# Kernel tuning notes

Hardware: AMD Instinct MI355X
Metric: run time of the kernel (lower is better)

## Reference

```python
import jax, jax.numpy as jnp
import numpy as np

B, T, H, Z0, D, MH = 1024, 256, 128, 64, 8, 256  # batch, time_steps, hidden, init_noise, data, mlp width


def _p(k, shape):
    s = 1.0 / np.sqrt(shape[0])
    return jax.random.uniform(k, shape, jnp.float32, -s, s)


def setup_inputs() -> dict:
    key = jax.random.key(0)
    ks = jax.random.split(key, 14)
    return {
        "init_noise": jax.random.normal(ks[0], (B, Z0), jnp.float32),
        "ts": jnp.arange(T, dtype=jnp.float32),
        "bm": jax.random.normal(ks[1], (T - 1, B, H), jnp.float32),  # standard normal; scaled by sqrt(dt)
        # initial embedding MLP: init_noise -> hidden state x0
        "iW1": _p(ks[2], (Z0, MH)), "ib1": jnp.zeros((MH,), jnp.float32),
        "iW2": _p(ks[3], (MH, H)), "ib2": jnp.zeros((H,), jnp.float32),
        # drift MLP (time dependent: input H+1)
        "fW1": _p(ks[4], (H + 1, MH)), "fb1": jnp.zeros((MH,), jnp.float32),
        "fW2": _p(ks[5], (MH, MH)), "fb2": jnp.zeros((MH,), jnp.float32),
        "fW3": _p(ks[6], (MH, H)), "fb3": jnp.zeros((H,), jnp.float32),
        # diffusion MLP (diagonal noise: output H)
        "gW1": _p(ks[7], (H + 1, MH)), "gb1": jnp.zeros((MH,), jnp.float32),
        "gW2": _p(ks[8], (MH, MH)), "gb2": jnp.zeros((MH,), jnp.float32),
        "gW3": _p(ks[9], (MH, H)), "gb3": jnp.zeros((H,), jnp.float32),
        # readout MLP: hidden -> data
        "rW1": _p(ks[10], (H, MH)), "rb1": jnp.zeros((MH,), jnp.float32),
        "rW2": _p(ks[11], (MH, D)), "rb2": jnp.zeros((D,), jnp.float32),
    }


def _mlp2(x, W1, b1, W2, b2):
    return jnp.tanh(x @ W1 + b1) @ W2 + b2


def _mlp3(x, W1, b1, W2, b2, W3, b3):
    h = jnp.tanh(x @ W1 + b1)
    h = jnp.tanh(h @ W2 + b2)
    return h @ W3 + b3


def reference(init_noise, ts, bm, iW1, ib1, iW2, ib2, fW1, fb1, fW2, fb2, fW3, fb3,
              gW1, gb1, gW2, gb2, gW3, gb3, rW1, rb1, rW2, rb2):
    dt = ts[1] - ts[0]
    sqdt = jnp.sqrt(dt)

    def f_and_g(t, x):
        # tx = cat([t, x], dim=1); time-dependent drift and diffusion
        tx = jnp.concatenate([jnp.full((x.shape[0], 1), t, x.dtype), x], axis=1)
        f = _mlp3(tx, fW1, fb1, fW2, fb2, fW3, fb3)
        g = _mlp3(tx, gW1, gb1, gW2, gb2, gW3, gb3)
        return f, g

    x0 = _mlp2(init_noise, iW1, ib1, iW2, ib2)  # [B, H]
    f0, g0 = f_and_g(ts[0], x0)

    def step(carry, inp):
        # reversible Heun (Stratonovich), as in torchsde 'reversible_heun'
        t1, z = inp
        y0, yh0, fp, gp = carry
        dW = z * sqdt  # Brownian increment ~ N(0, dt)
        yh1 = 2.0 * y0 - yh0 + fp * dt + gp * dW
        f1, g1 = f_and_g(t1, yh1)
        y1 = y0 + 0.5 * dt * (fp + f1) + 0.5 * (gp + g1) * dW
        return (y1, yh1, f1, g1), y1

    _, xs_rest = jax.lax.scan(step, (x0, x0, f0, g0), (ts[1:], bm))
    xs = jnp.concatenate([x0[None], xs_rest], axis=0).transpose(1, 0, 2)  # [B, T, H]
    ys = _mlp2(xs, rW1, rb1, rW2, rb2)  # [B, T, D]
    return ys
```

## Files before the change

kernel.cpp:

```cpp
#include <hip/hip_runtime.h>
#include <hip/hip_bf16.h>
#include <math.h>

#define NB  1024
#define T   256
#define H   128
#define Z0  64
#define D   8
#define MH  256

typedef __attribute__((ext_vector_type(8))) _Float16 half8;
typedef __attribute__((ext_vector_type(4))) _Float16 half4;
typedef __attribute__((ext_vector_type(4))) float f32x4;
typedef unsigned long long u64;

#define INV2048 4.8828125e-4f

#define OFF_F1 0
#define OFF_F2 64
#define OFF_F3 192
#define OFF_G1 256
#define OFF_G2 320
#define OFF_G3 448
#define OFF_R1 512
#define OFF_R2 576
#define OFF_I2 584
#define NFRAG  648

#define WS_HI16 0
#define WS_LO16 663552
#define WS_LO8  1327104
#define WS_EX   1658880
#define WS_FLG  4018176

#define KEEP(x) asm volatile("" : "+v"(x))

__device__ __forceinline__ f32x4 mfmaH(half8 a, half8 b, f32x4 c){
    return __builtin_amdgcn_mfma_f32_16x16x32_f16(a, b, c, 0, 0, 0);
}
__device__ __forceinline__ float ftanh(float x){
    float e = __expf(2.0f * x);
    return 1.0f - 2.0f * __builtin_amdgcn_rcpf(e + 1.0f);
}
__device__ __forceinline__ unsigned char f16_to_e5m2(_Float16 h){
    unsigned short hu = *reinterpret_cast<unsigned short*>(&h);
    return (unsigned char)((hu + 0x80) >> 8);
}
__device__ __forceinline__ half8 expandQ(u64 qw){
    unsigned int lo = (unsigned int)qw, hi = (unsigned int)(qw >> 32);
    union { unsigned int u[4]; half8 h; } u;
    u.u[0] = ((lo & 0xFFu) << 8) | ((lo & 0xFF00u) << 16);
    u.u[1] = ((lo >> 8) & 0xFF00u) | (lo & 0xFF000000u);
    u.u[2] = ((hi & 0xFFu) << 8) | ((hi & 0xFF00u) << 16);
    u.u[3] = ((hi >> 8) & 0xFF00u) | (hi & 0xFF000000u);
    return u.h;
}

__device__ __forceinline__ void st_sys4(float* p, f32x4 v){
    union { f32x4 v; u64 q[2]; } c; c.v = v;
    u64* d = reinterpret_cast<u64*>(p);
    __hip_atomic_store(d,     c.q[0], __ATOMIC_RELAXED, __HIP_MEMORY_SCOPE_SYSTEM);
    __hip_atomic_store(d + 1, c.q[1], __ATOMIC_RELAXED, __HIP_MEMORY_SCOPE_SYSTEM);
}
__device__ __forceinline__ f32x4 ld_sys4(float* p){
    union { u64 q[2]; f32x4 v; } c;
    u64* s = reinterpret_cast<u64*>(p);
    c.q[0] = __hip_atomic_load(s,     __ATOMIC_RELAXED, __HIP_MEMORY_SCOPE_SYSTEM);
    c.q[1] = __hip_atomic_load(s + 1, __ATOMIC_RELAXED, __HIP_MEMORY_SCOPE_SYSTEM);
    return c.v;
}
__device__ __forceinline__ void st_sys1(float* p, float v){
    union { float f; int i; } c; c.f = v;
    __hip_atomic_store(reinterpret_cast<int*>(p), c.i, __ATOMIC_RELAXED, __HIP_MEMORY_SCOPE_SYSTEM);
}
__device__ __forceinline__ float ld_sys1(float* p){
    union { int i; float f; } c;
    c.i = __hip_atomic_load(reinterpret_cast<int*>(p), __ATOMIC_RELAXED, __HIP_MEMORY_SCOPE_SYSTEM);
    return c.f;
}
__device__ __forceinline__ void flag_release_sys(int* p, int v){
    __hip_atomic_store(p, v, __ATOMIC_RELAXED, __HIP_MEMORY_SCOPE_SYSTEM);
}
__device__ __forceinline__ void flag_poll_sys(int* p, int v){
    while (__hip_atomic_load(p, __ATOMIC_RELAXED, __HIP_MEMORY_SCOPE_SYSTEM) < v)
        __builtin_amdgcn_s_sleep(2);
}

__device__ __forceinline__ half8 ldB(const _Float16* buf, int sb, int kt, int b, int q){
    const char* p = reinterpret_cast<const char*>(buf);
    return *reinterpret_cast<const half8*>(p + ((b*sb + kt*64 + q*16) ^ ((b & 7) << 4)));
}
__device__ __forceinline__ void stChunk(_Float16* buf, int sb, int b, int k0, half4 v){
    char* p = reinterpret_cast<char*>(buf);
    *reinterpret_cast<half4*>(p + ((b*sb + k0*2) ^ ((b & 7) << 4))) = v;
}
__device__ __forceinline__ void stOne(_Float16* buf, int sb, int b, int k, _Float16 v){
    char* p = reinterpret_cast<char*>(buf);
    *reinterpret_cast<_Float16*>(p + ((b*sb + k*2) ^ ((b & 7) << 4))) = v;
}
__device__ __forceinline__ u64 ldsQ(const char* base, int fragRel, int l){
    return *reinterpret_cast<const u64*>(base + fragRel*512 + l*8);
}

template<bool DOTANH>
__device__ __forceinline__ void storeOut(f32x4 m, f32x4 c, _Float16* Oh, _Float16* Ol, int b, int k0){
    half4 hh, ll;
    #pragma unroll
    for (int r = 0; r < 4; ++r){
        float v = m[r] + c[r]*INV2048;
        if (DOTANH) v = ftanh(v);
        _Float16 h = (_Float16)v;
        hh[r] = h;
        ll[r] = (_Float16)((v - (float)h)*2048.0f);
    }
    stChunk(Oh, 512, b, k0, hh);
    stChunk(Ol, 512, b, k0, ll);
}
__device__ __forceinline__ void storeA1(const float* v4, _Float16* Oh, _Float16* Ol, int b, int k0){
    half4 hh, ll;
    #pragma unroll
    for (int r = 0; r < 4; ++r){
        float v = v4[r];
        _Float16 h = (_Float16)v;
        hh[r] = h;
        ll[r] = (_Float16)((v - (float)h)*2048.0f);
    }
    stChunk(Oh, 256, b, k0, hh);
    stChunk(Ol, 256, b, k0, ll);
}
__device__ __forceinline__ void stOne2(_Float16* Oh, _Float16* Ol, int b, int k, float v){
    _Float16 h = (_Float16)v;
    stOne(Oh, 512, b, k, h);
    stOne(Ol, 512, b, k, (_Float16)((v - (float)h)*2048.0f));
}

template<int KT, bool DOTANH>
__device__ __forceinline__ void layerPairReg(
    const half8* Wh0, const half8* Wh1, const half8* Wl0, const half8* Wl1,
    const _Float16* Bh, const _Float16* Bl, int sbIn,
    _Float16* Oh, _Float16* Ol, const float* bias, int n0, int n1, int b, int q)
{
    f32x4 m0 = *reinterpret_cast<const f32x4*>(bias + n0*16 + 4*q);
    f32x4 m1 = *reinterpret_cast<const f32x4*>(bias + n1*16 + 4*q);
    f32x4 c0 = {0.f,0.f,0.f,0.f}, c1 = {0.f,0.f,0.f,0.f};
    #pragma unroll
    for (int kt = 0; kt < KT; ++kt){
        half8 bh = ldB(Bh, sbIn, kt, b, q);
        half8 bl = ldB(Bl, sbIn, kt, b, q);
        m0 = mfmaH(Wh0[kt], bh, m0);
        m1 = mfmaH(Wh1[kt], bh, m1);
        c0 = mfmaH(Wh0[kt], bl, c0);
        c1 = mfmaH(Wh1[kt], bl, c1);
        c0 = mfmaH(Wl0[kt], bh, c0);
        c1 = mfmaH(Wl1[kt], bh, c1);
    }
    storeOut<DOTANH>(m0, c0, Oh, Ol, b, n0*16 + 4*q);
    storeOut<DOTANH>(m1, c1, Oh, Ol, b, n1*16 + 4*q);
}
template<int KT, bool DOTANH>
__device__ __forceinline__ void layerPairLds(
    const half8* Wh0, const half8* Wh1, const char* WloLds, int f0, int f1, int l,
    const _Float16* Bh, const _Float16* Bl, int sbIn,
    _Float16* Oh, _Float16* Ol, const float* bias, int n0, int n1, int b, int q)
{
    f32x4 m0 = *reinterpret_cast<const f32x4*>(bias + n0*16 + 4*q);
    f32x4 m1 = *reinterpret_cast<const f32x4*>(bias + n1*16 + 4*q);
    f32x4 c0 = {0.f,0.f,0.f,0.f}, c1 = {0.f,0.f,0.f,0.f};
    #pragma unroll
    for (int kt = 0; kt < KT; ++kt){
        half8 bh = ldB(Bh, sbIn, kt, b, q);
        half8 bl = ldB(Bl, sbIn, kt, b, q);
        half8 w0l = expandQ(ldsQ(WloLds, f0 + kt, l));
        half8 w1l = expandQ(ldsQ(WloLds, f1 + kt, l));
        m0 = mfmaH(Wh0[kt], bh, m0);
        m1 = mfmaH(Wh1[kt], bh, m1);
        c0 = mfmaH(Wh0[kt], bl, c0);
        c1 = mfmaH(Wh1[kt], bl, c1);
        c0 = mfmaH(w0l, bh, c0);
        c1 = mfmaH(w1l, bh, c1);
    }
    storeOut<DOTANH>(m0, c0, Oh, Ol, b, n0*16 + 4*q);
    storeOut<DOTANH>(m1, c1, Oh, Ol, b, n1*16 + 4*q);
}
template<int KT>
__device__ __forceinline__ f32x4 layerOneLds(
    const half8* Wh, const char* WloLds, int f0, int l,
    const _Float16* Bh, const _Float16* Bl,
    const float* bias, int n0, int b, int q)
{
    f32x4 m = *reinterpret_cast<const f32x4*>(bias + n0*16 + 4*q);
    f32x4 c = {0.f,0.f,0.f,0.f};
    #pragma unroll
    for (int kt = 0; kt < KT; ++kt){
        half8 bh = ldB(Bh, 512, kt, b, q);
        half8 bl = ldB(Bl, 512, kt, b, q);
        half8 wl = expandQ(ldsQ(WloLds, f0 + kt, l));
        m = mfmaH(Wh[kt], bh, m);
        c = mfmaH(Wh[kt], bl, c);
        c = mfmaH(wl, bh, c);
    }
    #pragma unroll
    for (int r = 0; r < 4; ++r) m[r] += c[r]*INV2048;
    return m;
}

__global__ __launch_bounds__(64)
void pack_weights(const float* __restrict__ fW1, const float* __restrict__ fW2, const float* __restrict__ fW3,
                  const float* __restrict__ gW1, const float* __restrict__ gW2, const float* __restrict__ gW3,
                  const float* __restrict__ rW1, const float* __restrict__ rW2, const float* __restrict__ iW2,
                  unsigned char* __restrict__ ws)
{
    int f = blockIdx.x, l = threadIdx.x;
    const float* W; int KT, base, ld, ncols;
    if      (f <  64) { W = fW1+256; KT=4; base=OFF_F1; ld=256; ncols=256; }
    else if (f < 192) { W = fW2;     KT=8; base=OFF_F2; ld=256; ncols=256; }
    else if (f < 256) { W = fW3;     KT=8; base=OFF_F3; ld=128; ncols=128; }
    else if (f < 320) { W = gW1+256; KT=4; base=OFF_G1; ld=256; ncols=256; }
    else if (f < 448) { W = gW2;     KT=8; base=OFF_G2; ld=256; ncols=256; }
    else if (f < 512) { W = gW3;     KT=8; base=OFF_G3; ld=128; ncols=128; }
    else if (f < 576) { W = rW1;     KT=4; base=OFF_R1; ld=256; ncols=256; }
    else if (f < 584) { W = rW2;     KT=8; base=OFF_R2; ld=8;   ncols=8;   }
    else              { W = iW2;     KT=8; base=OFF_I2; ld=128; ncols=128; }
    int rel = f - base, n = rel / KT, kt = rel % KT;
    int krow = kt*32 + (l >> 4)*8;
    int col  = n*16  + (l & 15);
    half8 vh, vl; u64 qw = 0;
    #pragma unroll
    for (int j = 0; j < 8; ++j){
        float x = (col < ncols) ? W[(size_t)(krow + j)*ld + col] : 0.0f;
        _Float16 h = (_Float16)x;
        vh[j] = h;
        _Float16 r16 = (_Float16)((x - (float)h) * 2048.0f);
        vl[j] = r16;
        qw |= (u64)f16_to_e5m2(r16) << (8*j);
    }
    reinterpret_cast<half8*>(ws + WS_HI16)[(size_t)f*64 + l] = vh;
    reinterpret_cast<half8*>(ws + WS_LO16)[(size_t)f*64 + l] = vl;
    *reinterpret_cast<u64*>(ws + WS_LO8 + (size_t)f*512 + l*8) = qw;
}

__global__ __launch_bounds__(256)
void zero_flags(unsigned char* ws){
    int* fl = (int*)(ws + WS_FLG);
    #pragma unroll
    for (int i = 0; i < 16; ++i) fl[threadIdx.x + i*256] = 0;
}

__global__ __launch_bounds__(512, 2)
void sde_main(const float* __restrict__ init_noise, const float* __restrict__ ts,
              const float* __restrict__ bm,
              const float* __restrict__ iW1, const float* __restrict__ ib1,
              const float* __restrict__ ib2,
              const float* __restrict__ fb1, const float* __restrict__ fW1r,
              const float* __restrict__ fb2, const float* __restrict__ fb3,
              const float* __restrict__ gb1, const float* __restrict__ gW1r,
              const float* __restrict__ gb2, const float* __restrict__ gb3,
              const float* __restrict__ rb1, const float* __restrict__ rb2,
              unsigned char* __restrict__ ws,
              float* __restrict__ out)
{
    const int tid  = threadIdx.x;
    const int wv   = tid >> 6;
    const int l    = tid & 63;
    const int q    = l >> 4;
    const int b    = l & 15;
    const int bid  = blockIdx.x;
    const int role  = (bid >= 64) ? 1 : 0;
    const int group = bid & 63;
    const int row0  = group * 16;
    const int w8    = wv;

    __shared__ __align__(16) char Wlo2[65536];
    __shared__ __align__(16) char Wlo3[32768];
    __shared__ __align__(16) _Float16 A1h[16*128], A1l[16*128];
    __shared__ __align__(16) _Float16 H1h[16*256], H1l[16*256];
    __shared__ __align__(16) _Float16 H2h[16*256], H2l[16*256];
    __shared__ __align__(16) _Float16 Y1[16*128];
    __shared__ __align__(16) float part[512];
    __shared__ __align__(16) float s_b1[256];
    __shared__ __align__(16) float s_w1r0[256];
    __shared__ __align__(16) float s_bp[256];
    __shared__ __align__(16) float s_b2[256];
    __shared__ __align__(16) float s_b3[128];
    __shared__ __align__(16) float s_rb1h[128];
    __shared__ __align__(16) float s_rb2[8];

    const float* b1p = role ? gb1 : fb1;
    const float* w1p = role ? gW1r : fW1r;
    const float* b2p = role ? gb2 : fb2;
    const float* b3p = role ? gb3 : fb3;
    const int o1 = role ? OFF_G1 : OFF_F1;
    const int o2 = role ? OFF_G2 : OFF_F2;
    const int o3 = role ? OFF_G3 : OFF_F3;

    char* exg = (char*)ws + WS_EX + (size_t)group*36864;
    float* Xown = (float*)(exg + role*18432);
    float* Xpar = (float*)(exg + (1-role)*18432);
    int* flags   = (int*)(ws + WS_FLG + (size_t)group*256);
    int* flagOwn = flags + role;
    int* flagPar = flags + (1 - role);

    if (tid < 256){ s_b1[tid] = b1p[tid]; s_w1r0[tid] = w1p[tid]; s_b2[tid] = b2p[tid]; }
    else if (tid < 384){ s_b3[tid-256] = b3p[tid-256]; }
    else { s_rb1h[tid-384] = rb1[role*128 + (tid-384)]; }
    if (tid < 8) s_rb2[tid] = rb2[tid];
    float* zb = reinterpret_cast<float*>(H2h);
    zb[tid]       = init_noise[row0*Z0 + tid];
    zb[tid + 512] = init_noise[row0*Z0 + 512 + tid];
    {
        f32x4* d2 = (f32x4*)Wlo2; const f32x4* s2 = (const f32x4*)(ws + WS_LO8 + (size_t)o2*512);
        #pragma unroll
        for (int i = 0; i < 8; ++i) d2[tid + i*512] = s2[tid + i*512];
        f32x4* d3 = (f32x4*)Wlo3; const f32x4* s3 = (const f32x4*)(ws + WS_LO8 + (size_t)o3*512);
        #pragma unroll
        for (int i = 0; i < 4; ++i) d3[tid + i*512] = s3[tid + i*512];
    }
    const half8* hi  = reinterpret_cast<const half8*>(ws + WS_HI16);
    const half8* lo16 = reinterpret_cast<const half8*>(ws + WS_LO16);
    half8 W1h[2][4], W1l[2][4], W2h[2][8], W3h[8], WR1[4], WR2;
    #pragma unroll
    for (int kt = 0; kt < 4; ++kt){
        W1h[0][kt] = hi  [(size_t)(o1 + (2*w8  )*4 + kt)*64 + l];
        W1h[1][kt] = hi  [(size_t)(o1 + (2*w8+1)*4 + kt)*64 + l];
        W1l[0][kt] = lo16[(size_t)(o1 + (2*w8  )*4 + kt)*64 + l];
        W1l[1][kt] = lo16[(size_t)(o1 + (2*w8+1)*4 + kt)*64 + l];
        WR1[kt]    = hi  [(size_t)(OFF_R1 + (role*8 + w8)*4 + kt)*64 + l];
    }
    #pragma unroll
    for (int kt = 0; kt < 8; ++kt){
        W2h[0][kt] = hi[(size_t)(o2 + (2*w8  )*8 + kt)*64 + l];
        W2h[1][kt] = hi[(size_t)(o2 + (2*w8+1)*8 + kt)*64 + l];
        W3h[kt]    = hi[(size_t)(o3 + w8*8 + kt)*64 + l];
    }
    WR2 = hi[(size_t)(OFF_R2 + role*4 + (w8 & 3))*64 + l];

    #pragma unroll
    for (int s = 0; s < 2; ++s){
        #pragma unroll
        for (int kt = 0; kt < 4; ++kt){ KEEP(W1h[s][kt]); KEEP(W1l[s][kt]); }
        #pragma unroll
        for (int kt = 0; kt < 8; ++kt){ KEEP(W2h[s][kt]); }
    }
    #pragma unroll
    for (int kt = 0; kt < 8; ++kt){ KEEP(W3h[kt]); }
    __syncthreads();

    {
        const int c = tid & 255, hf = tid >> 8;
        float ac[8]; float bv = ib1[c];
        #pragma unroll
        for (int rr = 0; rr < 8; ++rr) ac[rr] = bv;
        for (int k = 0; k < Z0; ++k){
            float wt = iW1[k*256 + c];
            #pragma unroll
            for (int rr = 0; rr < 8; ++rr) ac[rr] += zb[(hf*8+rr)*Z0 + k] * wt;
        }
        #pragma unroll
        for (int rr = 0; rr < 8; ++rr) stOne2(H1h, H1l, hf*8+rr, c, ftanh(ac[rr]));
    }
    __syncthreads();

    float y[4], yh[4], fp[4], gp[4], bmv[4];
    {
        half8 ih[8], il[8];
        #pragma unroll
        for (int kt = 0; kt < 8; ++kt){
            ih[kt] = hi  [(size_t)(OFF_I2 + w8*8 + kt)*64 + l];
            il[kt] = lo16[(size_t)(OFF_I2 + w8*8 + kt)*64 + l];
        }
        f32x4 m = *reinterpret_cast<const f32x4*>(ib2 + w8*16 + 4*q);
        f32x4 c = {0.f,0.f,0.f,0.f};
        #pragma unroll
        for (int kt = 0; kt < 8; ++kt){
            half8 bh = ldB(H1h, 512, kt, b, q);
            half8 bl = ldB(H1l, 512, kt, b, q);
            m = mfmaH(ih[kt], bh, m);
            c = mfmaH(ih[kt], bl, c);
            c = mfmaH(il[kt], bh, c);
        }
        float xv[4]; half4 hv;
        #pragma unroll
        for (int r = 0; r < 4; ++r){
            float v = m[r] + c[r]*INV2048;
            y[r] = v; yh[r] = v; xv[r] = v; bmv[r] = 0.f;
            hv[r] = (_Float16)v;
        }
        storeA1(xv, A1h, A1l, b, w8*16 + 4*q);
        stChunk(Y1, 256, b, w8*16 + 4*q, hv);
    }

    const float ts0  = ts[0];
    const float dtv  = ts[1] - ts0;
    const float sqdt = sqrtf(dtv);

    #pragma unroll 1
    for (int t = 0; t < T; ++t){
        const float tval = ts0 + (float)t * dtv;
        const int par = t & 1;
        float dWv[4] = {0.f,0.f,0.f,0.f};
        if (t > 0){
            float nv[4];
            #pragma unroll
            for (int r = 0; r < 4; ++r){
                dWv[r] = bmv[r] * sqdt;
                float nyh = 2.0f*y[r] - yh[r] + fp[r]*dtv + gp[r]*dWv[r];
                yh[r] = nyh; nv[r] = nyh;
            }
            storeA1(nv, A1h, A1l, b, w8*16 + 4*q);
        }
        if (tid < 256) s_bp[tid] = s_b1[tid] + tval * s_w1r0[tid];
        __syncthreads();
        if (t < T-1){
            f32x4 bv = *reinterpret_cast<const f32x4*>(
                bm + (size_t)t*(NB*H) + (size_t)(row0+b)*H + w8*16 + 4*q);
            #pragma unroll
            for (int r = 0; r < 4; ++r) bmv[r] = bv[r];
        }
        layerPairReg<4, true>(W1h[0], W1h[1], W1l[0], W1l[1],
                              A1h, A1l, 256, H1h, H1l, s_bp, 2*w8, 2*w8+1, b, q);
        __syncthreads();
        layerPairLds<8, true>(W2h[0], W2h[1], Wlo2, (2*w8)*8, (2*w8+1)*8, l,
                              H1h, H1l, 512, H2h, H2l, s_b2, 2*w8, 2*w8+1, b, q);
        __syncthreads();
        f32x4 v3 = layerOneLds<8>(W3h, Wlo3, w8*8, l, H2h, H2l, s_b3, w8, b, q);
        st_sys4(Xown + par*2304 + (b*128 + w8*16 + 4*q), v3);
        {
            f32x4 m = *reinterpret_cast<const f32x4*>(s_rb1h + w8*16 + 4*q);
            #pragma unroll
            for (int kt = 0; kt < 4; ++kt) m = mfmaH(WR1[kt], ldB(Y1, 256, kt, b, q), m);
            half4 hv;
            #pragma unroll
            for (int r = 0; r < 4; ++r) hv[r] = (_Float16)ftanh(m[r]);
            stChunk(H1h, 512, b, w8*16 + 4*q, hv);
        }
        __syncthreads();
        {
            f32x4 pr = {0.f,0.f,0.f,0.f};
            pr = mfmaH(WR2, ldB(H1h, 512, (w8 & 3), b, q), pr);
            if (w8 < 4 && q < 2)
                *reinterpret_cast<f32x4*>(&part[((w8 & 3)*16 + b)*8 + 4*q]) = pr;
        }
        __syncthreads();
        float s_own = 0.f;
        if (tid < 128){
            #pragma unroll
            for (int p = 0; p < 4; ++p) s_own += part[p*128 + tid];
            st_sys1(Xown + par*2304 + 2048 + tid, s_own);
        }
        __syncthreads();
        if (tid == 0) flag_release_sys(flagOwn, t + 1);
        if (tid == 0) flag_poll_sys(flagPar, t + 1);
        __syncthreads();
        f32x4 vp = ld_sys4(Xpar + par*2304 + (b*128 + w8*16 + 4*q));
        {
            const int tr = t - 1;
            const bool writer = role ? (tid >= 64 && tid < 128) : (tid < 64);
            if (tr >= 0 && writer){
                float vo = s_own + ld_sys1(Xpar + par*2304 + 2048 + tid) + s_rb2[tid & 7];
                out[(size_t)(row0 + (tid >> 3))*(T*D) + (size_t)tr*D + (tid & 7)] = vo;
            }
        }
        {
            half4 hv;
            #pragma unroll
            for (int r = 0; r < 4; ++r){
                float fn = role ? vp[r] : v3[r];
                float gn = role ? v3[r] : vp[r];
                if (t > 0) y[r] += 0.5f*dtv*(fp[r] + fn) + 0.5f*(gp[r] + gn)*dWv[r];
                fp[r] = fn; gp[r] = gn;
                hv[r] = (_Float16)y[r];
            }
            stChunk(Y1, 256, b, w8*16 + 4*q, hv);
        }
    }

    __syncthreads();
    {
        f32x4 m = *reinterpret_cast<const f32x4*>(s_rb1h + w8*16 + 4*q);
        #pragma unroll
        for (int kt = 0; kt < 4; ++kt) m = mfmaH(WR1[kt], ldB(Y1, 256, kt, b, q), m);
        half4 hv;
        #pragma unroll
        for (int r = 0; r < 4; ++r) hv[r] = (_Float16)ftanh(m[r]);
        stChunk(H1h, 512, b, w8*16 + 4*q, hv);
    }
    __syncthreads();
    {
        f32x4 pr = {0.f,0.f,0.f,0.f};
        pr = mfmaH(WR2, ldB(H1h, 512, (w8 & 3), b, q), pr);
        if (w8 < 4 && q < 2)
            *reinterpret_cast<f32x4*>(&part[((w8 & 3)*16 + b)*8 + 4*q]) = pr;
    }
    __syncthreads();
    {
        const int par = T & 1;
        float s_own = 0.f;
        if (tid < 128){
            #pragma unroll
            for (int p = 0; p < 4; ++p) s_own += part[p*128 + tid];
            st_sys1(Xown + par*2304 + 2048 + tid, s_own);
        }
        __syncthreads();
        if (tid == 0) flag_release_sys(flagOwn, T + 1);
        if (tid == 0) flag_poll_sys(flagPar, T + 1);
        __syncthreads();
        const bool writer = role ? (tid >= 64 && tid < 128) : (tid < 64);
        if (writer){
            float vo = s_own + ld_sys1(Xpar + par*2304 + 2048 + tid) + s_rb2[tid & 7];
            out[(size_t)(row0 + (tid >> 3))*(T*D) + (size_t)(T-1)*D + (tid & 7)] = vo;
        }
    }
}

extern "C" void kernel_launch(void* const* d_in, const int* in_sizes, int n_in,
                              void* d_out, int out_size, void* d_ws, size_t ws_size,
                              hipStream_t stream)
{
    const float* init_noise = (const float*)d_in[0];
    const float* ts  = (const float*)d_in[1];
    const float* bm  = (const float*)d_in[2];
    const float* iW1 = (const float*)d_in[3];
    const float* ib1 = (const float*)d_in[4];
    const float* iW2 = (const float*)d_in[5];
    const float* ib2 = (const float*)d_in[6];
    const float* fW1 = (const float*)d_in[7];
    const float* fb1 = (const float*)d_in[8];
    const float* fW2 = (const float*)d_in[9];
    const float* fb2 = (const float*)d_in[10];
    const float* fW3 = (const float*)d_in[11];
    const float* fb3 = (const float*)d_in[12];
    const float* gW1 = (const float*)d_in[13];
    const float* gb1 = (const float*)d_in[14];
    const float* gW2 = (const float*)d_in[15];
    const float* gb2 = (const float*)d_in[16];
    const float* gW3 = (const float*)d_in[17];
    const float* gb3 = (const float*)d_in[18];
    const float* rW1 = (const float*)d_in[19];
    const float* rb1 = (const float*)d_in[20];
    const float* rW2 = (const float*)d_in[21];
    const float* rb2 = (const float*)d_in[22];

    unsigned char* ws = (unsigned char*)d_ws;

    zero_flags<<<dim3(1), dim3(256), 0, stream>>>(ws);
    pack_weights<<<dim3(NFRAG), dim3(64), 0, stream>>>(
        fW1, fW2, fW3, gW1, gW2, gW3, rW1, rW2, iW2, ws);
    sde_main<<<dim3(128), dim3(512), 0, stream>>>(
        init_noise, ts, bm, iW1, ib1, ib2,
        fb1, fW1, fb2, fb3,
        gb1, gW1, gb2, gb3,
        rb1, rb2, ws, (float*)d_out);
}
```

Before: 2.065 ms.

## Replace cross-block readout reduction with per-wave MFMA and global atomicAdd

The per-step readout no longer sums partial products in shared memory and exchanges them with the partner block through system-scope stores. Each wave now computes its readout contribution with its own rW2 fragment, repacked per wave, and adds it straight into the output with atomicAdd. A new prefill kernel writes rb2 into the output beforehand. This drops two __syncthreads and the partner readout exchange from each time step and shortens the flag poll sleep, at the cost of many float atomics to global memory and non-deterministic summation order.

```diff
diff --git a/kernel.cpp b/kernel.cpp
--- a/kernel.cpp
+++ b/kernel.cpp
@@ -69,21 +69,12 @@
     c.q[1] = __hip_atomic_load(s + 1, __ATOMIC_RELAXED, __HIP_MEMORY_SCOPE_SYSTEM);
     return c.v;
 }
-__device__ __forceinline__ void st_sys1(float* p, float v){
-    union { float f; int i; } c; c.f = v;
-    __hip_atomic_store(reinterpret_cast<int*>(p), c.i, __ATOMIC_RELAXED, __HIP_MEMORY_SCOPE_SYSTEM);
-}
-__device__ __forceinline__ float ld_sys1(float* p){
-    union { int i; float f; } c;
-    c.i = __hip_atomic_load(reinterpret_cast<int*>(p), __ATOMIC_RELAXED, __HIP_MEMORY_SCOPE_SYSTEM);
-    return c.f;
-}
 __device__ __forceinline__ void flag_release_sys(int* p, int v){
     __hip_atomic_store(p, v, __ATOMIC_RELAXED, __HIP_MEMORY_SCOPE_SYSTEM);
 }
 __device__ __forceinline__ void flag_poll_sys(int* p, int v){
     while (__hip_atomic_load(p, __ATOMIC_RELAXED, __HIP_MEMORY_SCOPE_SYSTEM) < v)
-        __builtin_amdgcn_s_sleep(2);
+        __builtin_amdgcn_s_sleep(1);
 }
 
 __device__ __forceinline__ half8 ldB(const _Float16* buf, int sb, int kt, int b, int q){
@@ -182,8 +173,7 @@
     storeOut<DOTANH>(m0, c0, Oh, Ol, b, n0*16 + 4*q);
     storeOut<DOTANH>(m1, c1, Oh, Ol, b, n1*16 + 4*q);
 }
-template<int KT>
-__device__ __forceinline__ f32x4 layerOneLds(
+__device__ __forceinline__ f32x4 layerOneLds8(
     const half8* Wh, const char* WloLds, int f0, int l,
     const _Float16* Bh, const _Float16* Bl,
     const float* bias, int n0, int b, int q)
@@ -191,7 +181,7 @@
     f32x4 m = *reinterpret_cast<const f32x4*>(bias + n0*16 + 4*q);
     f32x4 c = {0.f,0.f,0.f,0.f};
     #pragma unroll
-    for (int kt = 0; kt < KT; ++kt){
+    for (int kt = 0; kt < 8; ++kt){
         half8 bh = ldB(Bh, 512, kt, b, q);
         half8 bl = ldB(Bl, 512, kt, b, q);
         half8 wl = expandQ(ldsQ(WloLds, f0 + kt, l));
@@ -211,6 +201,21 @@
                   unsigned char* __restrict__ ws)
 {
     int f = blockIdx.x, l = threadIdx.x;
+    if (f >= OFF_R2 && f < OFF_I2){
+        int w8r = f - OFF_R2, d = l & 15, qq = l >> 4;
+        half8 v0, v1;
+        #pragma unroll
+        for (int j = 0; j < 8; ++j){
+            int kk = qq*8 + j;
+            bool ok = (d < 8) && (kk < 16);
+            v0[j] = ok ? (_Float16)rW2[(w8r*16 + kk)*8 + d]        : (_Float16)0.f;
+            v1[j] = ok ? (_Float16)rW2[(128 + w8r*16 + kk)*8 + d]  : (_Float16)0.f;
+        }
+        reinterpret_cast<half8*>(ws + WS_HI16)[(size_t)f*64 + l] = v0;
+        reinterpret_cast<half8*>(ws + WS_LO16)[(size_t)f*64 + l] = v1;
+        *reinterpret_cast<u64*>(ws + WS_LO8 + (size_t)f*512 + l*8) = 0ull;
+        return;
+    }
     const float* W; int KT, base, ld, ncols;
     if      (f <  64) { W = fW1+256; KT=4; base=OFF_F1; ld=256; ncols=256; }
     else if (f < 192) { W = fW2;     KT=8; base=OFF_F2; ld=256; ncols=256; }
@@ -219,7 +224,6 @@
     else if (f < 448) { W = gW2;     KT=8; base=OFF_G2; ld=256; ncols=256; }
     else if (f < 512) { W = gW3;     KT=8; base=OFF_G3; ld=128; ncols=128; }
     else if (f < 576) { W = rW1;     KT=4; base=OFF_R1; ld=256; ncols=256; }
-    else if (f < 584) { W = rW2;     KT=8; base=OFF_R2; ld=8;   ncols=8;   }
     else              { W = iW2;     KT=8; base=OFF_I2; ld=128; ncols=128; }
     int rel = f - base, n = rel / KT, kt = rel % KT;
     int krow = kt*32 + (l >> 4)*8;
@@ -244,6 +248,16 @@
     int* fl = (int*)(ws + WS_FLG);
     #pragma unroll
     for (int i = 0; i < 16; ++i) fl[threadIdx.x + i*256] = 0;
+}
+
+__global__ __launch_bounds__(256)
+void prefill_out(const float* __restrict__ rb2, float* __restrict__ out){
+    f32x4 v0, v1;
+    #pragma unroll
+    for (int r = 0; r < 4; ++r){ v0[r] = rb2[r]; v1[r] = rb2[4+r]; }
+    size_t i = ((size_t)blockIdx.x*256 + threadIdx.x)*2;
+    f32x4* o = reinterpret_cast<f32x4*>(out);
+    o[i] = v0; o[i+1] = v1;
 }
 
 __global__ __launch_bounds__(512, 2)
@@ -255,7 +269,7 @@
               const float* __restrict__ fb2, const float* __restrict__ fb3,
               const float* __restrict__ gb1, const float* __restrict__ gW1r,
               const float* __restrict__ gb2, const float* __restrict__ gb3,
-              const float* __restrict__ rb1, const float* __restrict__ rb2,
+              const float* __restrict__ rb1,
               unsigned char* __restrict__ ws,
               float* __restrict__ out)
 {
@@ -276,14 +290,13 @@
     __shared__ __align__(16) _Float16 H1h[16*256], H1l[16*256];
     __shared__ __align__(16) _Float16 H2h[16*256], H2l[16*256];
     __shared__ __align__(16) _Float16 Y1[16*128];
-    __shared__ __align__(16) float part[512];
+    __shared__ __align__(16) _Float16 Rb[8*256];
     __shared__ __align__(16) float s_b1[256];
     __shared__ __align__(16) float s_w1r0[256];
     __shared__ __align__(16) float s_bp[256];
     __shared__ __align__(16) float s_b2[256];
     __shared__ __align__(16) float s_b3[128];
     __shared__ __align__(16) float s_rb1h[128];
-    __shared__ __align__(16) float s_rb2[8];
 
     const float* b1p = role ? gb1 : fb1;
     const float* w1p = role ? gW1r : fW1r;
@@ -303,7 +316,6 @@
     if (tid < 256){ s_b1[tid] = b1p[tid]; s_w1r0[tid] = w1p[tid]; s_b2[tid] = b2p[tid]; }
     else if (tid < 384){ s_b3[tid-256] = b3p[tid-256]; }
     else { s_rb1h[tid-384] = rb1[role*128 + (tid-384)]; }
-    if (tid < 8) s_rb2[tid] = rb2[tid];
     float* zb = reinterpret_cast<float*>(H2h);
     zb[tid]       = init_noise[row0*Z0 + tid];
     zb[tid + 512] = init_noise[row0*Z0 + 512 + tid];
@@ -332,7 +344,7 @@
         W2h[1][kt] = hi[(size_t)(o2 + (2*w8+1)*8 + kt)*64 + l];
         W3h[kt]    = hi[(size_t)(o3 + w8*8 + kt)*64 + l];
     }
-    WR2 = hi[(size_t)(OFF_R2 + role*4 + (w8 & 3))*64 + l];
+    WR2 = role ? lo16[(size_t)(OFF_R2 + w8)*64 + l] : hi[(size_t)(OFF_R2 + w8)*64 + l];
 
     #pragma unroll
     for (int s = 0; s < 2; ++s){
@@ -422,44 +434,30 @@
         layerPairLds<8, true>(W2h[0], W2h[1], Wlo2, (2*w8)*8, (2*w8+1)*8, l,
                               H1h, H1l, 512, H2h, H2l, s_b2, 2*w8, 2*w8+1, b, q);
         __syncthreads();
-        f32x4 v3 = layerOneLds<8>(W3h, Wlo3, w8*8, l, H2h, H2l, s_b3, w8, b, q);
+        f32x4 v3 = layerOneLds8(W3h, Wlo3, w8*8, l, H2h, H2l, s_b3, w8, b, q);
         st_sys4(Xown + par*2304 + (b*128 + w8*16 + 4*q), v3);
-        {
+        f32x4 pr = {0.f,0.f,0.f,0.f};
+        if (t > 0){
             f32x4 m = *reinterpret_cast<const f32x4*>(s_rb1h + w8*16 + 4*q);
             #pragma unroll
             for (int kt = 0; kt < 4; ++kt) m = mfmaH(WR1[kt], ldB(Y1, 256, kt, b, q), m);
             half4 hv;
             #pragma unroll
             for (int r = 0; r < 4; ++r) hv[r] = (_Float16)ftanh(m[r]);
-            stChunk(H1h, 512, b, w8*16 + 4*q, hv);
-        }
-        __syncthreads();
-        {
-            f32x4 pr = {0.f,0.f,0.f,0.f};
-            pr = mfmaH(WR2, ldB(H1h, 512, (w8 & 3), b, q), pr);
-            if (w8 < 4 && q < 2)
-                *reinterpret_cast<f32x4*>(&part[((w8 & 3)*16 + b)*8 + 4*q]) = pr;
-        }
-        __syncthreads();
-        float s_own = 0.f;
-        if (tid < 128){
-            #pragma unroll
-            for (int p = 0; p < 4; ++p) s_own += part[p*128 + tid];
-            st_sys1(Xown + par*2304 + 2048 + tid, s_own);
+            *reinterpret_cast<half4*>(&Rb[w8*256 + b*16 + 4*q]) = hv;
+            half8 bf = *reinterpret_cast<const half8*>(&Rb[w8*256 + b*16 + (q&1)*8]);
+            pr = mfmaH(WR2, bf, pr);
         }
         __syncthreads();
         if (tid == 0) flag_release_sys(flagOwn, t + 1);
+        if (t > 0 && q < 2){
+            float* op = out + (size_t)(row0+b)*(T*D) + (size_t)(t-1)*D + 4*q;
+            #pragma unroll
+            for (int r = 0; r < 4; ++r) atomicAdd(op + r, pr[r]);
+        }
         if (tid == 0) flag_poll_sys(flagPar, t + 1);
         __syncthreads();
         f32x4 vp = ld_sys4(Xpar + par*2304 + (b*128 + w8*16 + 4*q));
-        {
-            const int tr = t - 1;
-            const bool writer = role ? (tid >= 64 && tid < 128) : (tid < 64);
-            if (tr >= 0 && writer){
-                float vo = s_own + ld_sys1(Xpar + par*2304 + 2048 + tid) + s_rb2[tid & 7];
-                out[(size_t)(row0 + (tid >> 3))*(T*D) + (size_t)tr*D + (tid & 7)] = vo;
-            }
-        }
         {
             half4 hv;
             #pragma unroll
@@ -482,32 +480,14 @@
         half4 hv;
         #pragma unroll
         for (int r = 0; r < 4; ++r) hv[r] = (_Float16)ftanh(m[r]);
-        stChunk(H1h, 512, b, w8*16 + 4*q, hv);
-    }
-    __syncthreads();
-    {
+        *reinterpret_cast<half4*>(&Rb[w8*256 + b*16 + 4*q]) = hv;
+        half8 bf = *reinterpret_cast<const half8*>(&Rb[w8*256 + b*16 + (q&1)*8]);
         f32x4 pr = {0.f,0.f,0.f,0.f};
-        pr = mfmaH(WR2, ldB(H1h, 512, (w8 & 3), b, q), pr);
-        if (w8 < 4 && q < 2)
-            *reinterpret_cast<f32x4*>(&part[((w8 & 3)*16 + b)*8 + 4*q]) = pr;
-    }
-    __syncthreads();
-    {
-        const int par = T & 1;
-        float s_own = 0.f;
-        if (tid < 128){
-            #pragma unroll
-            for (int p = 0; p < 4; ++p) s_own += part[p*128 + tid];
-            st_sys1(Xown + par*2304 + 2048 + tid, s_own);
-        }
-        __syncthreads();
-        if (tid == 0) flag_release_sys(flagOwn, T + 1);
-        if (tid == 0) flag_poll_sys(flagPar, T + 1);
-        __syncthreads();
-        const bool writer = role ? (tid >= 64 && tid < 128) : (tid < 64);
-        if (writer){
-            float vo = s_own + ld_sys1(Xpar + par*2304 + 2048 + tid) + s_rb2[tid & 7];
-            out[(size_t)(row0 + (tid >> 3))*(T*D) + (size_t)(T-1)*D + (tid & 7)] = vo;
+        pr = mfmaH(WR2, bf, pr);
+        if (q < 2){
+            float* op = out + (size_t)(row0+b)*(T*D) + (size_t)(T-1)*D + 4*q;
+            #pragma unroll
+            for (int r = 0; r < 4; ++r) atomicAdd(op + r, pr[r]);
         }
     }
 }
@@ -545,9 +525,10 @@
     zero_flags<<<dim3(1), dim3(256), 0, stream>>>(ws);
     pack_weights<<<dim3(NFRAG), dim3(64), 0, stream>>>(
         fW1, fW2, fW3, gW1, gW2, gW3, rW1, rW2, iW2, ws);
+    prefill_out<<<dim3(1024), dim3(256), 0, stream>>>(rb2, (float*)d_out);
     sde_main<<<dim3(128), dim3(512), 0, stream>>>(
         init_noise, ts, bm, iW1, ib1, ib2,
         fb1, fW1, fb2, fb3,
         gb1, gW1, gb2, gb3,
-        rb1, rb2, ws, (float*)d_out);
-}
+        rb1, ws, (float*)d_out);
+}
```

New measurement: 2.073 ms. Within noise of the previous version (+0.4%).
